# Kernel tuning notes

Hardware: AMD Instinct MI355X
Metric: run time of the kernel (lower is better)

Reference implementation:

```python
import jax, jax.numpy as jnp
import numpy as np
from jax import lax

B, L, N_NODES, N_SEQ = 256, 15360, 16, 64


def _lstm_layer(x, wih, whh, bih, bhh):
    # x: (B, T, I); torch gate order i, f, g, o
    H = whh.shape[1]
    b = bih + bhh
    def step(carry, xt):
        h, c = carry
        gates = xt @ wih.T + h @ whh.T + b
        i, f, g, o = jnp.split(gates, 4, axis=-1)
        c = jax.nn.sigmoid(f) * c + jax.nn.sigmoid(i) * jnp.tanh(g)
        h = jax.nn.sigmoid(o) * jnp.tanh(c)
        return (h, c), h
    h0 = jnp.zeros((x.shape[0], H), x.dtype)
    _, ys = lax.scan(step, (h0, h0), x.transpose(1, 0, 2))
    return ys.transpose(1, 0, 2)


def setup_inputs() -> dict:
    ks = iter(jax.random.split(jax.random.key(0), 64))
    def rn(shape, scale=1.0):
        return (jax.random.normal(next(ks), shape) * scale).astype(jnp.float32)
    d = {"x": rn((B, 1, L))}
    chs = [1, 16, 32, 64]
    for i in range(3):
        cin, cout = chs[i], chs[i + 1]
        s = 1.0 / np.sqrt(cin * 5)
        d[f"cw{i}"] = rn((cout, cin, 5), s)
        d[f"cb{i}"] = rn((cout,), s)
        d[f"bng{i}"] = jnp.ones((cout,), jnp.float32)
        d[f"bnb{i}"] = jnp.zeros((cout,), jnp.float32)
        d[f"bnm{i}"] = jnp.zeros((cout,), jnp.float32)
        d[f"bnv{i}"] = jnp.ones((cout,), jnp.float32)
    Hh = 64
    for l in range(2):
        s = 1.0 / np.sqrt(Hh)
        d[f"wih{l}"] = rn((4 * Hh, 64), s)
        d[f"whh{l}"] = rn((4 * Hh, Hh), s)
        d[f"bih{l}"] = rn((4 * Hh,), s)
        d[f"bhh{l}"] = rn((4 * Hh,), s)
    gin = [256, 64, 64]
    for l in range(3):
        s = 1.0 / np.sqrt(gin[l])
        d[f"gw{l}"] = rn((64, gin[l]), s)
        d[f"gb{l}"] = rn((64,), s)
    d["clw"] = rn((5, 64), 0.125)
    d["clb"] = rn((5,), 0.125)
    return d


def reference(x, cw0, cb0, bng0, bnb0, bnm0, bnv0, cw1, cb1, bng1, bnb1, bnm1, bnv1, cw2, cb2, bng2, bnb2, bnm2, bnv2, wih0, whh0, bih0, bhh0, wih1, whh1, bih1, bhh1, gw0, gb0, gw1, gb1, gw2, gb2, clw, clb):
    h = x
    # CNN: [Conv1d(k=5,p=2) -> BN(eval) -> ReLU -> MaxPool(2)] x 3
    for cw, cb, g, b, m, v in ((cw0, cb0, bng0, bnb0, bnm0, bnv0),
                               (cw1, cb1, bng1, bnb1, bnm1, bnv1),
                               (cw2, cb2, bng2, bnb2, bnm2, bnv2)):
        h = lax.conv_general_dilated(h, cw, (1,), [(2, 2)], dimension_numbers=("NCH", "OIH", "NCH")) + cb[None, :, None]
        h = g[None, :, None] * (h - m[None, :, None]) * lax.rsqrt(v[None, :, None] + 1e-5) + b[None, :, None]
        h = jax.nn.relu(h)
        Bq, Cq, Lq = h.shape
        h = h.reshape(Bq, Cq, Lq // 2, 2).max(-1)
    # AdaptiveAvgPool1d(64): length divisible by 64 -> exact mean bins
    Bq, Cq, Lq = h.shape
    h = h.reshape(Bq, Cq, N_SEQ, Lq // N_SEQ).mean(-1)
    h = h.transpose(0, 2, 1)  # (B, 64, 64) = (batch, seq, channels)
    # 2-layer LSTM (dropout is identity in eval)
    h = _lstm_layer(h, wih0, whh0, bih0, bhh0)
    h = _lstm_layer(h, wih1, whh1, bih1, bhh1)
    # Graph builder: Pearson-style correlation + value thresholding
    Hf = h.reshape(Bq, -1)
    fpn = Hf.shape[1] // N_NODES  # 256 features per node
    nf = Hf[:, :N_NODES * fpn].reshape(Bq, N_NODES, fpn)
    cen = nf - nf.mean(-1, keepdims=True)
    nrm = cen / (jnp.std(cen, axis=-1, ddof=1, keepdims=True) + 1e-8)
    C = jnp.einsum("bnf,bmf->bnm", nrm, nrm) / fpn  # (B, N, N)
    Cf = C.reshape(Bq, -1)
    k = min(max(1, int((100.0 - 25.0) / 100.0 * Cf.shape[1])), Cf.shape[1] - 1)
    thr = jnp.sort(Cf, axis=1)[:, k - 1]  # torch.kthvalue(k)
    eye = jnp.eye(N_NODES, dtype=C.dtype)
    adj = (C > thr[:, None, None]).astype(C.dtype) * (1.0 - eye)
    # GCN: x = ReLU(W (x + A x) + b), 3 layers, then max over nodes
    g = nf
    for gw, gb in ((gw0, gb0), (gw1, gb1), (gw2, gb2)):
        g = jax.nn.relu((g + jnp.einsum("bnm,bmf->bnf", adj, g)) @ gw.T + gb)
    emb = g.max(axis=1)
    return emb @ clw.T + clb
```

## Files before the change

### kernel.cpp

```cpp
#include <hip/hip_runtime.h>
#include <math.h>

typedef __attribute__((ext_vector_type(2))) float v2f;

__global__ __launch_bounds__(256) void prep_weights_kernel(
    const float* __restrict__ cw0, const float* __restrict__ cb0,
    const float* __restrict__ bng0, const float* __restrict__ bnb0,
    const float* __restrict__ bnm0, const float* __restrict__ bnv0,
    const float* __restrict__ cw1, const float* __restrict__ cb1,
    const float* __restrict__ bng1, const float* __restrict__ bnb1,
    const float* __restrict__ bnm1, const float* __restrict__ bnv1,
    const float* __restrict__ cw2, const float* __restrict__ cb2,
    const float* __restrict__ bng2, const float* __restrict__ bnb2,
    const float* __restrict__ bnm2, const float* __restrict__ bnv2,
    float* __restrict__ wt1, float* __restrict__ b1,
    float* __restrict__ wt2, float* __restrict__ b2,
    float* __restrict__ w0f, float* __restrict__ b0f)
{
    int tid = threadIdx.x;
    for (int i = tid; i < 2560; i += 256) {
        int co = i & 31, r = i >> 5, t = r % 5, ci = r / 5;
        float s = bng1[co] * rsqrtf(bnv1[co] + 1e-5f);
        wt1[i] = cw1[(co * 16 + ci) * 5 + t] * s;
    }
    if (tid < 32) {
        float s = bng1[tid] * rsqrtf(bnv1[tid] + 1e-5f);
        b1[tid] = (cb1[tid] - bnm1[tid]) * s + bnb1[tid];
    }
    for (int i = tid; i < 10240; i += 256) {
        int co = i & 63, r = i >> 6, t = r % 5, ci = r / 5;
        float s = bng2[co] * rsqrtf(bnv2[co] + 1e-5f);
        wt2[i] = cw2[(co * 32 + ci) * 5 + t] * s;
    }
    if (tid < 64) {
        float s = bng2[tid] * rsqrtf(bnv2[tid] + 1e-5f);
        b2[tid] = (cb2[tid] - bnm2[tid]) * s + bnb2[tid];
    }
    if (tid < 80) {
        int co = tid / 5;
        float s = bng0[co] * rsqrtf(bnv0[co] + 1e-5f);
        w0f[tid] = cw0[tid] * s;
    }
    if (tid < 16) {
        float s = bng0[tid] * rsqrtf(bnv0[tid] + 1e-5f);
        b0f[tid] = (cb0[tid] - bnm0[tid]) * s + bnb0[tid];
    }
}

__global__ __launch_bounds__(256) void convall_kernel(
    const float* __restrict__ x,
    const float* __restrict__ w0f, const float* __restrict__ b0f,
    const float* __restrict__ wt1, const float* __restrict__ b1,
    const float* __restrict__ wt2, const float* __restrict__ b2,
    float* __restrict__ xs)
{
    __shared__ float U[8096];
    float* raw = &U[4064];
    int b = blockIdx.y, bx = blockIdx.x, tid = threadIdx.x;
    const float* xb = x + (size_t)b * 15360;
    {
        int base = 480 * bx - 14;
        for (int i = tid; i < 508; i += 256) {
            int g = base + i;
            raw[i] = (g >= 0 && g < 15360) ? xb[g] : 0.f;
        }
    }
    __syncthreads();
    {
        int ci0 = tid >> 4, sub = tid & 15;
        float w0 = w0f[ci0*5+0], w1 = w0f[ci0*5+1], w2 = w0f[ci0*5+2],
              w3 = w0f[ci0*5+3], w4 = w0f[ci0*5+4];
        float bb = b0f[ci0];
        int r0g = 240 * bx - 6;
        for (int p = sub; p < 252; p += 16) {
            int r = r0g + p;
            float v = 0.f;
            if (r >= 0 && r < 7680) {
                int i0 = 2 * p;
                float c0 = raw[i0],   c1 = raw[i0+1], c2 = raw[i0+2],
                      c3 = raw[i0+3], c4 = raw[i0+4], c5 = raw[i0+5];
                float s0 = fmaf(w0,c0, fmaf(w1,c1, fmaf(w2,c2, fmaf(w3,c3, w4*c4))));
                float s1 = fmaf(w0,c1, fmaf(w1,c2, fmaf(w2,c3, fmaf(w3,c4, w4*c5))));
                v = fmaxf(fmaxf(s0, s1) + bb, 0.f);
            }
            U[ci0 * 254 + p] = v;
        }
    }
    __syncthreads();
    {
        int cg = tid >> 7, jj = tid & 127;
        int cgu = __builtin_amdgcn_readfirstlane(cg);
        if (tid < 64) { int co = tid >> 1, c = 124 + (tid & 1); U[4064 + co * 126 + c] = 0.f; }
        if (jj < 124) {
            const float* wb = wt1 + cgu * 16;
            v2f a0[8], a1[8];
#pragma unroll
            for (int q = 0; q < 8; ++q) { a0[q] = (v2f){0.f,0.f}; a1[q] = (v2f){0.f,0.f}; }
#pragma unroll 4
            for (int ci = 0; ci < 16; ++ci) {
                const float2* xr = reinterpret_cast<const float2*>(&U[ci * 254]);
                float2 xA = xr[jj], xB = xr[jj + 1], xC = xr[jj + 2];
                float xv[6] = { xA.x, xA.y, xB.x, xB.y, xC.x, xC.y };
#pragma unroll
                for (int t = 0; t < 5; ++t) {
                    const v2f* wp2 = reinterpret_cast<const v2f*>(wb + (ci * 5 + t) * 32);
                    v2f va = { xv[t], xv[t] };
                    v2f vc = { xv[t + 1], xv[t + 1] };
#pragma unroll
                    for (int q2 = 0; q2 < 8; ++q2) {
                        v2f w = wp2[q2];
                        a0[q2] = __builtin_elementwise_fma(w, va, a0[q2]);
                        a1[q2] = __builtin_elementwise_fma(w, vc, a1[q2]);
                    }
                }
            }
            int q = 120 * bx - 2 + jj;
            bool ok = (q >= 0 && q < 3840);
#pragma unroll
            for (int q2 = 0; q2 < 8; ++q2) {
#pragma unroll
                for (int cpp = 0; cpp < 2; ++cpp) {
                    int qq = 2 * q2 + cpp;
                    int co = cgu * 16 + qq;
                    float val = 0.f;
                    if (ok) val = fmaxf(fmaxf(a0[q2][cpp], a1[q2][cpp]) + b1[co], 0.f);
                    U[4064 + co * 126 + jj] = val;
                }
            }
        }
    }
    __syncthreads();
    {
        int cg = tid >> 6, jj = tid & 63;
        int jje = (jj < 59) ? jj : 59;
        int cgu = __builtin_amdgcn_readfirstlane(cg);
        const float* wb = wt2 + cgu * 16;
        v2f a0[8], a1[8];
#pragma unroll
        for (int q = 0; q < 8; ++q) { a0[q] = (v2f){0.f,0.f}; a1[q] = (v2f){0.f,0.f}; }
#pragma unroll 4
        for (int ci = 0; ci < 32; ++ci) {
            const float2* xr = reinterpret_cast<const float2*>(&U[4064 + ci * 126]);
            float2 xA = xr[jje], xB = xr[jje + 1], xC = xr[jje + 2];
            float xv[6] = { xA.x, xA.y, xB.x, xB.y, xC.x, xC.y };
#pragma unroll
            for (int t = 0; t < 5; ++t) {
                const v2f* wp2 = reinterpret_cast<const v2f*>(wb + (ci * 5 + t) * 64);
                v2f va = { xv[t], xv[t] };
                v2f vc = { xv[t + 1], xv[t + 1] };
#pragma unroll
                for (int q2 = 0; q2 < 8; ++q2) {
                    v2f w = wp2[q2];
                    a0[q2] = __builtin_elementwise_fma(w, va, a0[q2]);
                    a1[q2] = __builtin_elementwise_fma(w, vc, a1[q2]);
                }
            }
        }
        __syncthreads();
        if (jj < 60) {
#pragma unroll
            for (int q2 = 0; q2 < 8; ++q2) {
#pragma unroll
                for (int cpp = 0; cpp < 2; ++cpp) {
                    int qq = 2 * q2 + cpp;
                    int co = cgu * 16 + qq;
                    float m = fmaxf(a0[q2][cpp], a1[q2][cpp]) + b2[co];
                    U[co * 61 + jj] = fmaxf(m, 0.f);
                }
            }
        }
    }
    __syncthreads();
    if (tid < 128) {
        int co = tid & 63, bin = tid >> 6;
        const float* r = U + co * 61 + bin * 30;
        float s = 0.f;
#pragma unroll
        for (int k = 0; k < 30; ++k) s += r[k];
        xs[((size_t)b * 64 + (blockIdx.x * 2 + bin)) * 64 + co] = s * (1.f / 30.f);
    }
}

__global__ __launch_bounds__(256) void lstmgraph_kernel(
    const float* __restrict__ xseq,
    const float* __restrict__ wih0, const float* __restrict__ whh0,
    const float* __restrict__ bih0, const float* __restrict__ bhh0,
    const float* __restrict__ wih1, const float* __restrict__ whh1,
    const float* __restrict__ bih1, const float* __restrict__ bhh1,
    const float* __restrict__ gw0, const float* __restrict__ gb0,
    const float* __restrict__ gw1, const float* __restrict__ gb1,
    const float* __restrict__ gw2, const float* __restrict__ gb2,
    const float* __restrict__ clw, const float* __restrict__ clb,
    float* __restrict__ out)
{
    __shared__ float xb[64][64];
    __shared__ float xg[16384];
    __shared__ float gbuf[2][4][64];
    __shared__ float hbw[4][64];
    int b = blockIdx.x;
    int tid = threadIdx.x;
    int wv = tid >> 6, ln = tid & 63;
    for (int i = tid; i < 4096; i += 256) xb[i >> 6][i & 63] = xseq[(size_t)b * 4096 + i];
    __syncthreads();
    float wr[64];
    for (int layer = 0; layer < 2; ++layer) {
        const float* wih = layer ? wih1 : wih0;
        const float* whh = layer ? whh1 : whh0;
        float bias = layer ? (bih1[tid] + bhh1[tid]) : (bih0[tid] + bhh0[tid]);
#pragma unroll
        for (int k4 = 0; k4 < 16; ++k4) {
            float4 v = reinterpret_cast<const float4*>(wih + (size_t)tid * 64)[k4];
            wr[k4 * 4 + 0] = v.x; wr[k4 * 4 + 1] = v.y;
            wr[k4 * 4 + 2] = v.z; wr[k4 * 4 + 3] = v.w;
        }
        for (int t = 0; t < 64; ++t) {
            float s0 = bias, s1 = 0.f, s2 = 0.f, s3 = 0.f;
#pragma unroll
            for (int k4 = 0; k4 < 16; ++k4) {
                float4 xv4 = *reinterpret_cast<const float4*>(&xb[t][k4 * 4]);
                s0 = fmaf(wr[k4 * 4 + 0], xv4.x, s0);
                s1 = fmaf(wr[k4 * 4 + 1], xv4.y, s1);
                s2 = fmaf(wr[k4 * 4 + 2], xv4.z, s2);
                s3 = fmaf(wr[k4 * 4 + 3], xv4.w, s3);
            }
            xg[t * 256 + tid] = (s0 + s1) + (s2 + s3);
        }
#pragma unroll
        for (int k4 = 0; k4 < 16; ++k4) {
            float4 v = reinterpret_cast<const float4*>(whh + (size_t)tid * 64)[k4];
            wr[k4 * 4 + 0] = v.x; wr[k4 * 4 + 1] = v.y;
            wr[k4 * 4 + 2] = v.z; wr[k4 * 4 + 3] = v.w;
        }
        hbw[wv][ln] = 0.f;
        float c = 0.f;
        __syncthreads();
        for (int t = 0; t < 64; ++t) {
            float s0 = xg[t * 256 + tid], s1 = 0.f, s2 = 0.f, s3 = 0.f;
#pragma unroll
            for (int k4 = 0; k4 < 16; ++k4) {
                float4 hv4 = *reinterpret_cast<const float4*>(&hbw[wv][k4 * 4]);
                s0 = fmaf(wr[k4 * 4 + 0], hv4.x, s0);
                s1 = fmaf(wr[k4 * 4 + 1], hv4.y, s1);
                s2 = fmaf(wr[k4 * 4 + 2], hv4.z, s2);
                s3 = fmaf(wr[k4 * 4 + 3], hv4.w, s3);
            }
            float acc = (s0 + s1) + (s2 + s3);
            float a;
            if (wv == 2) a = tanhf(acc);
            else         a = 1.f / (1.f + __expf(-acc));
            gbuf[t & 1][wv][ln] = a;
            __syncthreads();
            float gi = gbuf[t & 1][0][ln], gf = gbuf[t & 1][1][ln],
                  gg = gbuf[t & 1][2][ln], go = gbuf[t & 1][3][ln];
            c = fmaf(gf, c, gi * gg);
            float h = go * tanhf(c);
            hbw[wv][ln] = h;
            if (wv == 0) xb[t][ln] = h;
        }
        __syncthreads();
    }
    float* nf   = xg;
    float* sb   = xg + 4112;
    float* red  = xg + 8224;
    float* mean = xg + 8496;
    float* rstd = xg + 8512;
    float* C    = xg + 8528;
    float* adj  = xg + 8784;
    float* thrv = xg + 9040;
    float* bufA = xg + 9044;
    float* bufB = xg + 10084;
    float* bufC = xg + 11124;
    float* emb  = xg + 12164;
    for (int i = tid; i < 4096; i += 256) {
        int n = i >> 8, f = i & 255;
        nf[n * 257 + f] = xb[4 * n + (f >> 6)][f & 63];
    }
    __syncthreads();
    int nd = tid >> 4, sub = tid & 15;
    {
        float s = 0.f;
        for (int f = sub; f < 256; f += 16) s += nf[nd * 257 + f];
        red[nd * 17 + sub] = s;
    }
    __syncthreads();
    if (tid < 16) {
        float m = 0.f;
        for (int i = 0; i < 16; ++i) m += red[tid * 17 + i];
        mean[tid] = m * (1.f / 256.f);
    }
    __syncthreads();
    {
        float mu = mean[nd];
        float ss = 0.f;
        for (int f = sub; f < 256; f += 16) { float d = nf[nd * 257 + f] - mu; ss = fmaf(d, d, ss); }
        red[nd * 17 + sub] = ss;
    }
    __syncthreads();
    if (tid < 16) {
        float m = 0.f;
        for (int i = 0; i < 16; ++i) m += red[tid * 17 + i];
        rstd[tid] = 1.f / (sqrtf(m * (1.f / 255.f)) + 1e-8f);
    }
    __syncthreads();
    for (int i = tid; i < 4096; i += 256) {
        int n = i >> 8, f = i & 255;
        sb[n * 257 + f] = (nf[n * 257 + f] - mean[n]) * rstd[n];
    }
    __syncthreads();
    {
        int n = tid >> 4, m = tid & 15;
        float a0 = 0, a1 = 0, a2 = 0, a3 = 0;
        for (int f = 0; f < 256; f += 4) {
            a0 = fmaf(sb[n * 257 + f + 0], sb[m * 257 + f + 0], a0);
            a1 = fmaf(sb[n * 257 + f + 1], sb[m * 257 + f + 1], a1);
            a2 = fmaf(sb[n * 257 + f + 2], sb[m * 257 + f + 2], a2);
            a3 = fmaf(sb[n * 257 + f + 3], sb[m * 257 + f + 3], a3);
        }
        C[tid] = ((a0 + a1) + (a2 + a3)) * (1.f / 256.f);
    }
    __syncthreads();
    {
        float v = C[tid];
        int cnt = 0, eq = 0;
        for (int j2 = 0; j2 < 256; ++j2) {
            float vj = C[j2];
            cnt += (vj < v);
            eq  += (vj == v);
        }
        if (cnt <= 191 && 191 < cnt + eq) thrv[0] = v;
    }
    __syncthreads();
    {
        int n = tid >> 4, m = tid & 15;
        adj[tid] = (C[tid] > thrv[0] && n != m) ? 1.f : 0.f;
    }
    __syncthreads();
    for (int i = tid; i < 4096; i += 256) {
        int n = i >> 8, f = i & 255;
        float acc = nf[n * 257 + f];
#pragma unroll
        for (int m = 0; m < 16; ++m) acc = fmaf(adj[n * 16 + m], nf[m * 257 + f], acc);
        sb[n * 257 + f] = acc;
    }
    __syncthreads();
    for (int i = tid; i < 1024; i += 256) {
        int n = i >> 6, o = i & 63;
        const float4* wr4 = reinterpret_cast<const float4*>(gw0 + (size_t)o * 256);
        float acc = gb0[o];
        for (int f4 = 0; f4 < 64; ++f4) {
            float4 wv4 = wr4[f4];
            int f = f4 * 4;
            acc = fmaf(sb[n * 257 + f + 0], wv4.x, acc);
            acc = fmaf(sb[n * 257 + f + 1], wv4.y, acc);
            acc = fmaf(sb[n * 257 + f + 2], wv4.z, acc);
            acc = fmaf(sb[n * 257 + f + 3], wv4.w, acc);
        }
        bufA[n * 65 + o] = fmaxf(acc, 0.f);
    }
    __syncthreads();
    for (int i = tid; i < 1024; i += 256) {
        int n = i >> 6, f = i & 63;
        float acc = bufA[n * 65 + f];
#pragma unroll
        for (int m = 0; m < 16; ++m) acc = fmaf(adj[n * 16 + m], bufA[m * 65 + f], acc);
        bufB[n * 65 + f] = acc;
    }
    __syncthreads();
    for (int i = tid; i < 1024; i += 256) {
        int n = i >> 6, o = i & 63;
        const float4* wr4 = reinterpret_cast<const float4*>(gw1 + (size_t)o * 64);
        float acc = gb1[o];
        for (int f4 = 0; f4 < 16; ++f4) {
            float4 wv4 = wr4[f4];
            int f = f4 * 4;
            acc = fmaf(bufB[n * 65 + f + 0], wv4.x, acc);
            acc = fmaf(bufB[n * 65 + f + 1], wv4.y, acc);
            acc = fmaf(bufB[n * 65 + f + 2], wv4.z, acc);
            acc = fmaf(bufB[n * 65 + f + 3], wv4.w, acc);
        }
        bufC[n * 65 + o] = fmaxf(acc, 0.f);
    }
    __syncthreads();
    for (int i = tid; i < 1024; i += 256) {
        int n = i >> 6, f = i & 63;
        float acc = bufC[n * 65 + f];
#pragma unroll
        for (int m = 0; m < 16; ++m) acc = fmaf(adj[n * 16 + m], bufC[m * 65 + f], acc);
        bufA[n * 65 + f] = acc;
    }
    __syncthreads();
    for (int i = tid; i < 1024; i += 256) {
        int n = i >> 6, o = i & 63;
        const float4* wr4 = reinterpret_cast<const float4*>(gw2 + (size_t)o * 64);
        float acc = gb2[o];
        for (int f4 = 0; f4 < 16; ++f4) {
            float4 wv4 = wr4[f4];
            int f = f4 * 4;
            acc = fmaf(bufA[n * 65 + f + 0], wv4.x, acc);
            acc = fmaf(bufA[n * 65 + f + 1], wv4.y, acc);
            acc = fmaf(bufA[n * 65 + f + 2], wv4.z, acc);
            acc = fmaf(bufA[n * 65 + f + 3], wv4.w, acc);
        }
        bufB[n * 65 + o] = fmaxf(acc, 0.f);
    }
    __syncthreads();
    if (tid < 64) {
        float mx = bufB[0 * 65 + tid];
#pragma unroll
        for (int n = 1; n < 16; ++n) mx = fmaxf(mx, bufB[n * 65 + tid]);
        emb[tid] = mx;
    }
    __syncthreads();
    if (tid < 5) {
        float acc = clb[tid];
#pragma unroll
        for (int o = 0; o < 64; ++o) acc = fmaf(emb[o], clw[tid * 64 + o], acc);
        out[(size_t)b * 5 + tid] = acc;
    }
}

extern "C" void kernel_launch(void* const* d_in, const int* in_sizes, int n_in,
                              void* d_out, int out_size, void* d_ws, size_t ws_size,
                              hipStream_t stream)
{
    const float* x    = (const float*)d_in[0];
    const float* cw0  = (const float*)d_in[1];
    const float* cb0  = (const float*)d_in[2];
    const float* bng0 = (const float*)d_in[3];
    const float* bnb0 = (const float*)d_in[4];
    const float* bnm0 = (const float*)d_in[5];
    const float* bnv0 = (const float*)d_in[6];
    const float* cw1  = (const float*)d_in[7];
    const float* cb1  = (const float*)d_in[8];
    const float* bng1 = (const float*)d_in[9];
    const float* bnb1 = (const float*)d_in[10];
    const float* bnm1 = (const float*)d_in[11];
    const float* bnv1 = (const float*)d_in[12];
    const float* cw2  = (const float*)d_in[13];
    const float* cb2  = (const float*)d_in[14];
    const float* bng2 = (const float*)d_in[15];
    const float* bnb2 = (const float*)d_in[16];
    const float* bnm2 = (const float*)d_in[17];
    const float* bnv2 = (const float*)d_in[18];
    const float* wih0 = (const float*)d_in[19];
    const float* whh0 = (const float*)d_in[20];
    const float* bih0 = (const float*)d_in[21];
    const float* bhh0 = (const float*)d_in[22];
    const float* wih1 = (const float*)d_in[23];
    const float* whh1 = (const float*)d_in[24];
    const float* bih1 = (const float*)d_in[25];
    const float* bhh1 = (const float*)d_in[26];
    const float* gw0  = (const float*)d_in[27];
    const float* gb0  = (const float*)d_in[28];
    const float* gw1  = (const float*)d_in[29];
    const float* gb1  = (const float*)d_in[30];
    const float* gw2  = (const float*)d_in[31];
    const float* gb2  = (const float*)d_in[32];
    const float* clw  = (const float*)d_in[33];
    const float* clb  = (const float*)d_in[34];

    float* xs  = (float*)d_ws;
    float* wt1 = xs + 1048576;
    float* b1  = wt1 + 2560;
    float* wt2 = b1 + 32;
    float* b2  = wt2 + 10240;
    float* w0f = b2 + 64;
    float* b0f = w0f + 80;

    prep_weights_kernel<<<1, 256, 0, stream>>>(
        cw0, cb0, bng0, bnb0, bnm0, bnv0,
        cw1, cb1, bng1, bnb1, bnm1, bnv1,
        cw2, cb2, bng2, bnb2, bnm2, bnv2,
        wt1, b1, wt2, b2, w0f, b0f);
    convall_kernel<<<dim3(32, 256), 256, 0, stream>>>(x, w0f, b0f, wt1, b1, wt2, b2, xs);
    lstmgraph_kernel<<<256, 256, 0, stream>>>(xs, wih0, whh0, bih0, bhh0,
                                              wih1, whh1, bih1, bhh1,
                                              gw0, gb0, gw1, gb1, gw2, gb2,
                                              clw, clb, (float*)d_out);
}
```

Before: 469.0 us.

## Fuse LSTM layer-0 input projection into conv kernel and restructure LSTM kernel

Layer-0 input-gate projection is now computed inside the conv kernel, which has abundant parallelism, and written to global memory as precomputed gate inputs. The LSTM kernel drops its large shared xg buffer, streams gate inputs from global with one-step prefetch, and uses 512 threads so the layer-1 input projection is split across two halves of the block. Weights are pre-transposed into a coalesced float4 layout by a now multi-block prep kernel. The cost is 32 MB of extra global traffic for the xg buffers, and half the threads sit idle during the recurrent loops.

```diff
diff --git a/kernel.cpp b/kernel.cpp
--- a/kernel.cpp
+++ b/kernel.cpp
@@ -13,37 +13,50 @@
     const float* __restrict__ cw2, const float* __restrict__ cb2,
     const float* __restrict__ bng2, const float* __restrict__ bnb2,
     const float* __restrict__ bnm2, const float* __restrict__ bnv2,
+    const float* __restrict__ wih0, const float* __restrict__ whh0,
+    const float* __restrict__ wih1, const float* __restrict__ whh1,
     float* __restrict__ wt1, float* __restrict__ b1,
     float* __restrict__ wt2, float* __restrict__ b2,
-    float* __restrict__ w0f, float* __restrict__ b0f)
+    float* __restrict__ w0f, float* __restrict__ b0f,
+    float* __restrict__ wih0c, float* __restrict__ whh0c,
+    float* __restrict__ wih1c, float* __restrict__ whh1c)
 {
-    int tid = threadIdx.x;
-    for (int i = tid; i < 2560; i += 256) {
+    int g = blockIdx.x * 256 + threadIdx.x;
+    const int GS = 64 * 256;
+    for (int i = g; i < 2560; i += GS) {
         int co = i & 31, r = i >> 5, t = r % 5, ci = r / 5;
         float s = bng1[co] * rsqrtf(bnv1[co] + 1e-5f);
         wt1[i] = cw1[(co * 16 + ci) * 5 + t] * s;
     }
-    if (tid < 32) {
-        float s = bng1[tid] * rsqrtf(bnv1[tid] + 1e-5f);
-        b1[tid] = (cb1[tid] - bnm1[tid]) * s + bnb1[tid];
-    }
-    for (int i = tid; i < 10240; i += 256) {
+    if (g < 32) {
+        float s = bng1[g] * rsqrtf(bnv1[g] + 1e-5f);
+        b1[g] = (cb1[g] - bnm1[g]) * s + bnb1[g];
+    }
+    for (int i = g; i < 10240; i += GS) {
         int co = i & 63, r = i >> 6, t = r % 5, ci = r / 5;
         float s = bng2[co] * rsqrtf(bnv2[co] + 1e-5f);
         wt2[i] = cw2[(co * 32 + ci) * 5 + t] * s;
     }
-    if (tid < 64) {
-        float s = bng2[tid] * rsqrtf(bnv2[tid] + 1e-5f);
-        b2[tid] = (cb2[tid] - bnm2[tid]) * s + bnb2[tid];
-    }
-    if (tid < 80) {
-        int co = tid / 5;
+    if (g < 64) {
+        float s = bng2[g] * rsqrtf(bnv2[g] + 1e-5f);
+        b2[g] = (cb2[g] - bnm2[g]) * s + bnb2[g];
+    }
+    if (g < 80) {
+        int co = g / 5;
         float s = bng0[co] * rsqrtf(bnv0[co] + 1e-5f);
-        w0f[tid] = cw0[tid] * s;
-    }
-    if (tid < 16) {
-        float s = bng0[tid] * rsqrtf(bnv0[tid] + 1e-5f);
-        b0f[tid] = (cb0[tid] - bnm0[tid]) * s + bnb0[tid];
+        w0f[g] = cw0[g] * s;
+    }
+    if (g < 16) {
+        float s = bng0[g] * rsqrtf(bnv0[g] + 1e-5f);
+        b0f[g] = (cb0[g] - bnm0[g]) * s + bnb0[g];
+    }
+    for (int i = g; i < 16384; i += GS) {
+        int c = i & 3, r = (i >> 2) & 255, k4 = i >> 10;
+        int src = r * 64 + k4 * 4 + c;
+        wih0c[i] = wih0[src];
+        whh0c[i] = whh0[src];
+        wih1c[i] = wih1[src];
+        whh1c[i] = whh1[src];
     }
 }
 
@@ -52,7 +65,9 @@
     const float* __restrict__ w0f, const float* __restrict__ b0f,
     const float* __restrict__ wt1, const float* __restrict__ b1,
     const float* __restrict__ wt2, const float* __restrict__ b2,
-    float* __restrict__ xs)
+    const float* __restrict__ wih0c,
+    const float* __restrict__ bih0, const float* __restrict__ bhh0,
+    float* __restrict__ xg0g)
 {
     __shared__ float U[8096];
     float* raw = &U[4064];
@@ -177,15 +192,39 @@
         float s = 0.f;
 #pragma unroll
         for (int k = 0; k < 30; ++k) s += r[k];
-        xs[((size_t)b * 64 + (blockIdx.x * 2 + bin)) * 64 + co] = s * (1.f / 30.f);
+        U[3904 + bin * 64 + co] = s * (1.f / 30.f);
+    }
+    __syncthreads();
+    {
+        int r = tid;
+        float bias0 = bih0[r] + bhh0[r];
+        float wr0[64];
+#pragma unroll
+        for (int k4 = 0; k4 < 16; ++k4) {
+            float4 w4 = reinterpret_cast<const float4*>(wih0c)[k4 * 256 + r];
+            wr0[k4*4+0] = w4.x; wr0[k4*4+1] = w4.y;
+            wr0[k4*4+2] = w4.z; wr0[k4*4+3] = w4.w;
+        }
+#pragma unroll
+        for (int bin = 0; bin < 2; ++bin) {
+            float s0 = bias0, s1 = 0.f, s2 = 0.f, s3 = 0.f;
+#pragma unroll
+            for (int k4 = 0; k4 < 16; ++k4) {
+                float4 xv4 = *reinterpret_cast<const float4*>(&U[3904 + bin * 64 + k4 * 4]);
+                s0 = fmaf(wr0[k4*4+0], xv4.x, s0);
+                s1 = fmaf(wr0[k4*4+1], xv4.y, s1);
+                s2 = fmaf(wr0[k4*4+2], xv4.z, s2);
+                s3 = fmaf(wr0[k4*4+3], xv4.w, s3);
+            }
+            xg0g[((size_t)b * 64 + 2 * bx + bin) * 256 + r] = (s0 + s1) + (s2 + s3);
+        }
     }
 }
 
-__global__ __launch_bounds__(256) void lstmgraph_kernel(
-    const float* __restrict__ xseq,
-    const float* __restrict__ wih0, const float* __restrict__ whh0,
-    const float* __restrict__ bih0, const float* __restrict__ bhh0,
-    const float* __restrict__ wih1, const float* __restrict__ whh1,
+__global__ __launch_bounds__(512) void lstmgraph_kernel(
+    const float* __restrict__ xg0g, float* __restrict__ xg1g,
+    const float* __restrict__ whh0c, const float* __restrict__ wih1c,
+    const float* __restrict__ whh1c,
     const float* __restrict__ bih1, const float* __restrict__ bhh1,
     const float* __restrict__ gw0, const float* __restrict__ gb0,
     const float* __restrict__ gw1, const float* __restrict__ gb1,
@@ -194,90 +233,143 @@
     float* __restrict__ out)
 {
     __shared__ float xb[64][64];
-    __shared__ float xg[16384];
-    __shared__ float gbuf[2][4][64];
-    __shared__ float hbw[4][64];
+    __shared__ float G[12228];
+    float* gbuf = G;
+    float* hbw  = G + 512;
     int b = blockIdx.x;
     int tid = threadIdx.x;
     int wv = tid >> 6, ln = tid & 63;
-    for (int i = tid; i < 4096; i += 256) xb[i >> 6][i & 63] = xseq[(size_t)b * 4096 + i];
-    __syncthreads();
+    size_t base0 = (size_t)b * 16384;
     float wr[64];
-    for (int layer = 0; layer < 2; ++layer) {
-        const float* wih = layer ? wih1 : wih0;
-        const float* whh = layer ? whh1 : whh0;
-        float bias = layer ? (bih1[tid] + bhh1[tid]) : (bih0[tid] + bhh0[tid]);
+    if (wv < 4) {
 #pragma unroll
         for (int k4 = 0; k4 < 16; ++k4) {
-            float4 v = reinterpret_cast<const float4*>(wih + (size_t)tid * 64)[k4];
-            wr[k4 * 4 + 0] = v.x; wr[k4 * 4 + 1] = v.y;
-            wr[k4 * 4 + 2] = v.z; wr[k4 * 4 + 3] = v.w;
-        }
-        for (int t = 0; t < 64; ++t) {
-            float s0 = bias, s1 = 0.f, s2 = 0.f, s3 = 0.f;
+            float4 w4 = reinterpret_cast<const float4*>(whh0c)[k4 * 256 + tid];
+            wr[k4*4+0] = w4.x; wr[k4*4+1] = w4.y;
+            wr[k4*4+2] = w4.z; wr[k4*4+3] = w4.w;
+        }
+        hbw[wv * 64 + ln] = 0.f;
+    }
+    float c = 0.f;
+    float xg_cur = (wv < 4) ? xg0g[base0 + tid] : 0.f;
+    for (int t = 0; t < 64; ++t) {
+        float xg_nxt = 0.f;
+        if (wv < 4 && t < 63) xg_nxt = xg0g[base0 + (size_t)(t + 1) * 256 + tid];
+        if (wv < 4) {
+            float s0 = xg_cur, s1 = 0.f, s2 = 0.f, s3 = 0.f;
 #pragma unroll
             for (int k4 = 0; k4 < 16; ++k4) {
-                float4 xv4 = *reinterpret_cast<const float4*>(&xb[t][k4 * 4]);
-                s0 = fmaf(wr[k4 * 4 + 0], xv4.x, s0);
-                s1 = fmaf(wr[k4 * 4 + 1], xv4.y, s1);
-                s2 = fmaf(wr[k4 * 4 + 2], xv4.z, s2);
-                s3 = fmaf(wr[k4 * 4 + 3], xv4.w, s3);
-            }
-            xg[t * 256 + tid] = (s0 + s1) + (s2 + s3);
-        }
-#pragma unroll
-        for (int k4 = 0; k4 < 16; ++k4) {
-            float4 v = reinterpret_cast<const float4*>(whh + (size_t)tid * 64)[k4];
-            wr[k4 * 4 + 0] = v.x; wr[k4 * 4 + 1] = v.y;
-            wr[k4 * 4 + 2] = v.z; wr[k4 * 4 + 3] = v.w;
-        }
-        hbw[wv][ln] = 0.f;
-        float c = 0.f;
-        __syncthreads();
-        for (int t = 0; t < 64; ++t) {
-            float s0 = xg[t * 256 + tid], s1 = 0.f, s2 = 0.f, s3 = 0.f;
-#pragma unroll
-            for (int k4 = 0; k4 < 16; ++k4) {
-                float4 hv4 = *reinterpret_cast<const float4*>(&hbw[wv][k4 * 4]);
-                s0 = fmaf(wr[k4 * 4 + 0], hv4.x, s0);
-                s1 = fmaf(wr[k4 * 4 + 1], hv4.y, s1);
-                s2 = fmaf(wr[k4 * 4 + 2], hv4.z, s2);
-                s3 = fmaf(wr[k4 * 4 + 3], hv4.w, s3);
+                float4 hv4 = *reinterpret_cast<const float4*>(&hbw[wv * 64 + k4 * 4]);
+                s0 = fmaf(wr[k4*4+0], hv4.x, s0);
+                s1 = fmaf(wr[k4*4+1], hv4.y, s1);
+                s2 = fmaf(wr[k4*4+2], hv4.z, s2);
+                s3 = fmaf(wr[k4*4+3], hv4.w, s3);
             }
             float acc = (s0 + s1) + (s2 + s3);
             float a;
             if (wv == 2) a = tanhf(acc);
             else         a = 1.f / (1.f + __expf(-acc));
-            gbuf[t & 1][wv][ln] = a;
-            __syncthreads();
-            float gi = gbuf[t & 1][0][ln], gf = gbuf[t & 1][1][ln],
-                  gg = gbuf[t & 1][2][ln], go = gbuf[t & 1][3][ln];
+            gbuf[(t & 1) * 256 + wv * 64 + ln] = a;
+        }
+        __syncthreads();
+        if (wv < 4) {
+            float gi = gbuf[(t & 1) * 256 + 0 * 64 + ln], gf = gbuf[(t & 1) * 256 + 1 * 64 + ln],
+                  gg = gbuf[(t & 1) * 256 + 2 * 64 + ln], go = gbuf[(t & 1) * 256 + 3 * 64 + ln];
             c = fmaf(gf, c, gi * gg);
             float h = go * tanhf(c);
-            hbw[wv][ln] = h;
+            hbw[wv * 64 + ln] = h;
             if (wv == 0) xb[t][ln] = h;
         }
+        xg_cur = xg_nxt;
+    }
+    __syncthreads();
+    {
+        int r = tid & 255;
+        int tb = (tid >> 8) * 32;
+        float bias1 = bih1[r] + bhh1[r];
+        float wr1[64];
+#pragma unroll
+        for (int k4 = 0; k4 < 16; ++k4) {
+            float4 w4 = reinterpret_cast<const float4*>(wih1c)[k4 * 256 + r];
+            wr1[k4*4+0] = w4.x; wr1[k4*4+1] = w4.y;
+            wr1[k4*4+2] = w4.z; wr1[k4*4+3] = w4.w;
+        }
+        for (int tt = 0; tt < 32; ++tt) {
+            int t = tb + tt;
+            float s0 = bias1, s1 = 0.f, s2 = 0.f, s3 = 0.f;
+#pragma unroll
+            for (int k4 = 0; k4 < 16; ++k4) {
+                float4 xv4 = *reinterpret_cast<const float4*>(&xb[t][k4 * 4]);
+                s0 = fmaf(wr1[k4*4+0], xv4.x, s0);
+                s1 = fmaf(wr1[k4*4+1], xv4.y, s1);
+                s2 = fmaf(wr1[k4*4+2], xv4.z, s2);
+                s3 = fmaf(wr1[k4*4+3], xv4.w, s3);
+            }
+            xg1g[base0 + (size_t)t * 256 + r] = (s0 + s1) + (s2 + s3);
+        }
+    }
+    if (wv < 4) {
+#pragma unroll
+        for (int k4 = 0; k4 < 16; ++k4) {
+            float4 w4 = reinterpret_cast<const float4*>(whh1c)[k4 * 256 + tid];
+            wr[k4*4+0] = w4.x; wr[k4*4+1] = w4.y;
+            wr[k4*4+2] = w4.z; wr[k4*4+3] = w4.w;
+        }
+        hbw[wv * 64 + ln] = 0.f;
+    }
+    c = 0.f;
+    __syncthreads();
+    xg_cur = (wv < 4) ? xg1g[base0 + tid] : 0.f;
+    for (int t = 0; t < 64; ++t) {
+        float xg_nxt = 0.f;
+        if (wv < 4 && t < 63) xg_nxt = xg1g[base0 + (size_t)(t + 1) * 256 + tid];
+        if (wv < 4) {
+            float s0 = xg_cur, s1 = 0.f, s2 = 0.f, s3 = 0.f;
+#pragma unroll
+            for (int k4 = 0; k4 < 16; ++k4) {
+                float4 hv4 = *reinterpret_cast<const float4*>(&hbw[wv * 64 + k4 * 4]);
+                s0 = fmaf(wr[k4*4+0], hv4.x, s0);
+                s1 = fmaf(wr[k4*4+1], hv4.y, s1);
+                s2 = fmaf(wr[k4*4+2], hv4.z, s2);
+                s3 = fmaf(wr[k4*4+3], hv4.w, s3);
+            }
+            float acc = (s0 + s1) + (s2 + s3);
+            float a;
+            if (wv == 2) a = tanhf(acc);
+            else         a = 1.f / (1.f + __expf(-acc));
+            gbuf[(t & 1) * 256 + wv * 64 + ln] = a;
+        }
         __syncthreads();
-    }
-    float* nf   = xg;
-    float* sb   = xg + 4112;
-    float* red  = xg + 8224;
-    float* mean = xg + 8496;
-    float* rstd = xg + 8512;
-    float* C    = xg + 8528;
-    float* adj  = xg + 8784;
-    float* thrv = xg + 9040;
-    float* bufA = xg + 9044;
-    float* bufB = xg + 10084;
-    float* bufC = xg + 11124;
-    float* emb  = xg + 12164;
-    for (int i = tid; i < 4096; i += 256) {
+        if (wv < 4) {
+            float gi = gbuf[(t & 1) * 256 + 0 * 64 + ln], gf = gbuf[(t & 1) * 256 + 1 * 64 + ln],
+                  gg = gbuf[(t & 1) * 256 + 2 * 64 + ln], go = gbuf[(t & 1) * 256 + 3 * 64 + ln];
+            c = fmaf(gf, c, gi * gg);
+            float h = go * tanhf(c);
+            hbw[wv * 64 + ln] = h;
+            if (wv == 0) xb[t][ln] = h;
+        }
+        xg_cur = xg_nxt;
+    }
+    __syncthreads();
+    float* nf   = G;
+    float* sb   = G + 4112;
+    float* red  = G + 8224;
+    float* mean = G + 8496;
+    float* rstd = G + 8512;
+    float* C    = G + 8528;
+    float* adj  = G + 8784;
+    float* thrv = G + 9040;
+    float* bufA = G + 9044;
+    float* bufB = G + 10084;
+    float* bufC = G + 11124;
+    float* emb  = G + 12164;
+    for (int i = tid; i < 4096; i += 512) {
         int n = i >> 8, f = i & 255;
         nf[n * 257 + f] = xb[4 * n + (f >> 6)][f & 63];
     }
     __syncthreads();
-    int nd = tid >> 4, sub = tid & 15;
-    {
+    int nd = (tid >> 4) & 15, sub = tid & 15;
+    if (tid < 256) {
         float s = 0.f;
         for (int f = sub; f < 256; f += 16) s += nf[nd * 257 + f];
         red[nd * 17 + sub] = s;
@@ -289,7 +381,7 @@
         mean[tid] = m * (1.f / 256.f);
     }
     __syncthreads();
-    {
+    if (tid < 256) {
         float mu = mean[nd];
         float ss = 0.f;
         for (int f = sub; f < 256; f += 16) { float d = nf[nd * 257 + f] - mu; ss = fmaf(d, d, ss); }
@@ -302,12 +394,12 @@
         rstd[tid] = 1.f / (sqrtf(m * (1.f / 255.f)) + 1e-8f);
     }
     __syncthreads();
-    for (int i = tid; i < 4096; i += 256) {
+    for (int i = tid; i < 4096; i += 512) {
         int n = i >> 8, f = i & 255;
         sb[n * 257 + f] = (nf[n * 257 + f] - mean[n]) * rstd[n];
     }
     __syncthreads();
-    {
+    if (tid < 256) {
         int n = tid >> 4, m = tid & 15;
         float a0 = 0, a1 = 0, a2 = 0, a3 = 0;
         for (int f = 0; f < 256; f += 4) {
@@ -319,7 +411,7 @@
         C[tid] = ((a0 + a1) + (a2 + a3)) * (1.f / 256.f);
     }
     __syncthreads();
-    {
+    if (tid < 256) {
         float v = C[tid];
         int cnt = 0, eq = 0;
         for (int j2 = 0; j2 < 256; ++j2) {
@@ -330,12 +422,12 @@
         if (cnt <= 191 && 191 < cnt + eq) thrv[0] = v;
     }
     __syncthreads();
-    {
+    if (tid < 256) {
         int n = tid >> 4, m = tid & 15;
         adj[tid] = (C[tid] > thrv[0] && n != m) ? 1.f : 0.f;
     }
     __syncthreads();
-    for (int i = tid; i < 4096; i += 256) {
+    for (int i = tid; i < 4096; i += 512) {
         int n = i >> 8, f = i & 255;
         float acc = nf[n * 257 + f];
 #pragma unroll
@@ -343,7 +435,7 @@
         sb[n * 257 + f] = acc;
     }
     __syncthreads();
-    for (int i = tid; i < 1024; i += 256) {
+    for (int i = tid; i < 1024; i += 512) {
         int n = i >> 6, o = i & 63;
         const float4* wr4 = reinterpret_cast<const float4*>(gw0 + (size_t)o * 256);
         float acc = gb0[o];
@@ -358,7 +450,7 @@
         bufA[n * 65 + o] = fmaxf(acc, 0.f);
     }
     __syncthreads();
-    for (int i = tid; i < 1024; i += 256) {
+    for (int i = tid; i < 1024; i += 512) {
         int n = i >> 6, f = i & 63;
         float acc = bufA[n * 65 + f];
 #pragma unroll
@@ -366,7 +458,7 @@
         bufB[n * 65 + f] = acc;
     }
     __syncthreads();
-    for (int i = tid; i < 1024; i += 256) {
+    for (int i = tid; i < 1024; i += 512) {
         int n = i >> 6, o = i & 63;
         const float4* wr4 = reinterpret_cast<const float4*>(gw1 + (size_t)o * 64);
         float acc = gb1[o];
@@ -381,7 +473,7 @@
         bufC[n * 65 + o] = fmaxf(acc, 0.f);
     }
     __syncthreads();
-    for (int i = tid; i < 1024; i += 256) {
+    for (int i = tid; i < 1024; i += 512) {
         int n = i >> 6, f = i & 63;
         float acc = bufC[n * 65 + f];
 #pragma unroll
@@ -389,7 +481,7 @@
         bufA[n * 65 + f] = acc;
     }
     __syncthreads();
-    for (int i = tid; i < 1024; i += 256) {
+    for (int i = tid; i < 1024; i += 512) {
         int n = i >> 6, o = i & 63;
         const float4* wr4 = reinterpret_cast<const float4*>(gw2 + (size_t)o * 64);
         float acc = gb2[o];
@@ -405,7 +497,7 @@
     }
     __syncthreads();
     if (tid < 64) {
-        float mx = bufB[0 * 65 + tid];
+        float mx = bufB[tid];
 #pragma unroll
         for (int n = 1; n < 16; ++n) mx = fmaxf(mx, bufB[n * 65 + tid]);
         emb[tid] = mx;
@@ -459,22 +551,29 @@
     const float* clw  = (const float*)d_in[33];
     const float* clb  = (const float*)d_in[34];
 
-    float* xs  = (float*)d_ws;
-    float* wt1 = xs + 1048576;
-    float* b1  = wt1 + 2560;
-    float* wt2 = b1 + 32;
-    float* b2  = wt2 + 10240;
-    float* w0f = b2 + 64;
-    float* b0f = w0f + 80;
-
-    prep_weights_kernel<<<1, 256, 0, stream>>>(
+    float* xg0   = (float*)d_ws;
+    float* xg1   = xg0 + 4194304;
+    float* wt1   = xg1 + 4194304;
+    float* b1    = wt1 + 2560;
+    float* wt2   = b1 + 32;
+    float* b2    = wt2 + 10240;
+    float* w0f   = b2 + 64;
+    float* b0f   = w0f + 80;
+    float* wih0c = b0f + 16;
+    float* whh0c = wih0c + 16384;
+    float* wih1c = whh0c + 16384;
+    float* whh1c = wih1c + 16384;
+
+    prep_weights_kernel<<<64, 256, 0, stream>>>(
         cw0, cb0, bng0, bnb0, bnm0, bnv0,
         cw1, cb1, bng1, bnb1, bnm1, bnv1,
         cw2, cb2, bng2, bnb2, bnm2, bnv2,
-        wt1, b1, wt2, b2, w0f, b0f);
-    convall_kernel<<<dim3(32, 256), 256, 0, stream>>>(x, w0f, b0f, wt1, b1, wt2, b2, xs);
-    lstmgraph_kernel<<<256, 256, 0, stream>>>(xs, wih0, whh0, bih0, bhh0,
-                                              wih1, whh1, bih1, bhh1,
-                                              gw0, gb0, gw1, gb1, gw2, gb2,
-                                              clw, clb, (float*)d_out);
+        wih0, whh0, wih1, whh1,
+        wt1, b1, wt2, b2, w0f, b0f,
+        wih0c, whh0c, wih1c, whh1c);
+    convall_kernel<<<dim3(32, 256), 256, 0, stream>>>(
+        x, w0f, b0f, wt1, b1, wt2, b2, wih0c, bih0, bhh0, xg0);
+    lstmgraph_kernel<<<256, 512, 0, stream>>>(
+        xg0, xg1, whh0c, wih1c, whh1c, bih1, bhh1,
+        gw0, gb0, gw1, gb1, gw2, gb2, clw, clb, (float*)d_out);
 }
```

Measured after the change: 462.4 us. Within noise of the previous version (-1.4%).
